# Optimization experiments

Hardware: AMD Instinct MI355X
Metric: run time of the kernel (lower is better)

The kernel has to match this reference:

```python
import jax, jax.numpy as jnp
import numpy as np

N = 20000          # nodes
E = 200000         # edges
IN = 256           # in_channels
OUT = 256          # out_channels (heads * per-head)
H = 2              # heads
C = OUT // 2       # per-head channels (out_channels // 2)
TDIM = 100         # time_enc.out_channels
MSG = 156          # msg_dim
EDGE_DIM = TDIM + MSG  # 256
P = 0.1            # dropout prob


def setup_inputs() -> dict:
    key = jax.random.key(0)
    ks = jax.random.split(key, 20)
    s = 1.0 / np.sqrt(IN)
    se = 1.0 / np.sqrt(EDGE_DIM)
    return {
        "x": jax.random.normal(ks[0], (N, IN), jnp.float32),
        "last_update": jax.random.uniform(ks[1], (N,), jnp.float32) * 100.0,
        "edge_index": jax.random.randint(ks[2], (2, E), 0, N, jnp.int64),
        "t": jax.random.uniform(ks[3], (E,), jnp.float32) * 100.0,
        "msg": jax.random.normal(ks[4], (E, MSG), jnp.float32),
        "u_edge": jax.random.uniform(ks[5], (E,), jnp.float32),
        "u_attn": jax.random.uniform(ks[6], (E, H), jnp.float32),
        # TimeEncoder: cos(Linear(1, TDIM))
        "time_w": jax.random.normal(ks[7], (TDIM,), jnp.float32),
        "time_b": jax.random.normal(ks[8], (TDIM,), jnp.float32) * 0.1,
        # TransformerConv params ([in, out] layout)
        "Wq": jax.random.normal(ks[9], (IN, H * C), jnp.float32) * s,
        "bq": jnp.zeros((H * C,), jnp.float32),
        "Wk": jax.random.normal(ks[10], (IN, H * C), jnp.float32) * s,
        "bk": jnp.zeros((H * C,), jnp.float32),
        "Wv": jax.random.normal(ks[11], (IN, H * C), jnp.float32) * s,
        "bv": jnp.zeros((H * C,), jnp.float32),
        "We": jax.random.normal(ks[12], (EDGE_DIM, H * C), jnp.float32) * se,
        "be": jnp.zeros((H * C,), jnp.float32),
        "Ws": jax.random.normal(ks[13], (IN, H * C), jnp.float32) * s,
        "bs": jnp.zeros((H * C,), jnp.float32),
    }


def reference(x, last_update, edge_index, t, msg, u_edge, u_attn,
              time_w, time_b, Wq, bq, Wk, bk, Wv, bv, We, be, Ws, bs):
    src, dst = edge_index[0], edge_index[1]
    # time encoding of relative time (TGN TimeEncoder: cos(Linear(1, TDIM)))
    rel_t = last_update[src] - t                              # [E]
    rel_enc = jnp.cos(rel_t[:, None] * time_w[None, :] + time_b)  # [E, TDIM]
    edge_attr = jnp.concatenate([rel_enc, msg], axis=-1)      # [E, EDGE_DIM]
    # dropout_adj: drop edges with prob P (no rescale)
    keep = u_edge > P                                         # [E] bool

    q = (x @ Wq + bq).reshape(N, H, C)
    k = (x @ Wk + bk).reshape(N, H, C)
    v = (x @ Wv + bv).reshape(N, H, C)
    e = (edge_attr @ We + be).reshape(E, H, C)

    kj = k[src] + e                                           # [E, H, C]
    alpha = jnp.einsum('ehc,ehc->eh', q[dst], kj) / jnp.sqrt(jnp.float32(C))
    alpha = jnp.where(keep[:, None], alpha, -jnp.inf)
    # segment softmax over incoming edges of each dst node
    m = jax.ops.segment_max(alpha, dst, num_segments=N)       # [N, H]
    m = jnp.where(jnp.isfinite(m), m, 0.0)
    ex = jnp.where(keep[:, None], jnp.exp(alpha - m[dst]), 0.0)
    denom = jax.ops.segment_sum(ex, dst, num_segments=N)      # [N, H]
    attn = ex / (denom[dst] + 1e-16)                          # [E, H]
    # attention dropout (post-softmax, inverted scaling)
    attn = attn * (u_attn > P).astype(attn.dtype) / (1.0 - P)

    msg_out = (v[src] + e) * attn[:, :, None]                 # [E, H, C]
    out = jax.ops.segment_sum(msg_out, dst, num_segments=N).reshape(N, H * C)
    # root/skip connection
    return out + (x @ Ws + bs)
```

## Files before the change

kernel.cpp:

```cpp
#include <hip/hip_runtime.h>

#define NND 20000
#define NE 200000
#define PDROP 0.1f

typedef unsigned short u16;
typedef __bf16 bf16x8 __attribute__((ext_vector_type(8)));
typedef float f32x4 __attribute__((ext_vector_type(4)));

__device__ __forceinline__ float b2f(u16 u) {
  unsigned v = ((unsigned)u) << 16;
  float f;
  __builtin_memcpy(&f, &v, 4);
  return f;
}
__device__ __forceinline__ u16 f2b(float f) {
  unsigned x;
  __builtin_memcpy(&x, &f, 4);
  unsigned r = x + 0x7fffu + ((x >> 16) & 1u);
  return (u16)(r >> 16);
}

__global__ void convert_x(const float* __restrict__ x, u16* __restrict__ xb) {
  int i = blockIdx.x * blockDim.x + threadIdx.x;
  if (i < NND * 256 / 4) {
    float4 v = ((const float4*)x)[i];
    ushort4 o;
    o.x = f2b(v.x); o.y = f2b(v.y); o.z = f2b(v.z); o.w = f2b(v.w);
    ((ushort4*)xb)[i] = o;
  }
}

struct WTArgs {
  const float* W[6];
  u16* WT[6];
};
__global__ void convert_wT(WTArgs a) {
  int gid = blockIdx.x * blockDim.x + threadIdx.x;
  if (gid >= 6 * 65536) return;
  int w = gid >> 16, r = gid & 65535;
  if (w < 5) {
    int n = r >> 8, k = r & 255;
    a.WT[w][n * 256 + k] = f2b(a.W[w][k * 256 + n]);
  } else {
    a.WT[5][r] = f2b(a.W[5][r]);
  }
}

__global__ void zero2(int* __restrict__ cnt, int* __restrict__ cur) {
  int i = blockIdx.x * blockDim.x + threadIdx.x;
  if (i < NND) { cnt[i] = 0; cur[i] = 0; }
}
__global__ void csr_count(const int* __restrict__ ei, int* __restrict__ cnt) {
  int e = blockIdx.x * blockDim.x + threadIdx.x;
  if (e < NE) atomicAdd(&cnt[ei[NE + e]], 1);
}
__global__ __launch_bounds__(1024) void scan_rowptr(const int* __restrict__ cnt,
                                                    int* __restrict__ rowptr) {
  __shared__ int sums[1024];
  const int tid = threadIdx.x;
  const int base = tid * 20;
  int local[20];
  int run = 0;
#pragma unroll
  for (int i = 0; i < 20; i++) {
    int idx = base + i;
    local[i] = run;
    run += (idx < NND) ? cnt[idx] : 0;
  }
  sums[tid] = run;
  __syncthreads();
  for (int off = 1; off < 1024; off <<= 1) {
    int v = (tid >= off) ? sums[tid - off] : 0;
    __syncthreads();
    sums[tid] += v;
    __syncthreads();
  }
  int prev = (tid > 0) ? sums[tid - 1] : 0;
#pragma unroll
  for (int i = 0; i < 20; i++) {
    int idx = base + i;
    if (idx < NND) rowptr[idx] = prev + local[i];
  }
  if (tid == 1023) rowptr[NND] = sums[1023];
}
__global__ void csr_fill(const int* __restrict__ ei,
                         const float* __restrict__ last_update,
                         const float* __restrict__ t,
                         const float* __restrict__ u_edge,
                         const float* __restrict__ u_attn,
                         const int* __restrict__ rowptr, int* __restrict__ cur,
                         int* __restrict__ elist, uint4* __restrict__ recs) {
  int e = blockIdx.x * blockDim.x + threadIdx.x;
  if (e < NE) {
    int s = ei[e];
    int d = ei[NE + e];
    int p = rowptr[d] + atomicAdd(&cur[d], 1);
    elist[p] = e;
    bool keep = u_edge[e] > PDROP;
    float rt = last_update[s] - t[e];
    float2 ua = *(const float2*)&u_attn[(size_t)e * 2];
    uint4 r;
    r.x = (unsigned)s | (keep ? 0u : 0x80000000u);
    r.y = __float_as_uint(rt);
    r.z = __float_as_uint(ua.x > PDROP ? (1.f / 0.9f) : 0.f);
    r.w = __float_as_uint(ua.y > PDROP ? (1.f / 0.9f) : 0.f);
    recs[p] = r;
  }
}

__device__ __forceinline__ void mfma_tile(const u16 (*As)[72], const u16 (*Bs)[72],
                                          f32x4 acc[4][4], int wm, int wn,
                                          int fr, int fg) {
#pragma unroll
  for (int ks = 0; ks < 2; ks++) {
    bf16x8 a[4], b[4];
#pragma unroll
    for (int i = 0; i < 4; i++)
      a[i] = *(const bf16x8*)&As[wm * 64 + i * 16 + fr][ks * 32 + fg * 8];
#pragma unroll
    for (int j = 0; j < 4; j++)
      b[j] = *(const bf16x8*)&Bs[wn * 64 + j * 16 + fr][ks * 32 + fg * 8];
#pragma unroll
    for (int i = 0; i < 4; i++)
#pragma unroll
      for (int j = 0; j < 4; j++)
        acc[i][j] = __builtin_amdgcn_mfma_f32_16x16x32_bf16(a[i], b[j], acc[i][j], 0, 0, 0);
  }
}

struct NodeArgs {
  const u16* BT[4];
  const float* bias[4];
  u16* outb[3];
  float* outf;
};
__global__ __launch_bounds__(256) void gemm_node(const u16* __restrict__ xb,
                                                 NodeArgs args) {
  __shared__ __attribute__((aligned(16))) u16 As[128][72];
  __shared__ __attribute__((aligned(16))) u16 Bs[128][72];
  const int tid = threadIdx.x;
  const int w = blockIdx.y >> 1;
  const int col0 = (blockIdx.y & 1) * 128;
  const int row0 = blockIdx.x * 128;
  const u16* BT = args.BT[w];
  const float* bias = args.bias[w];
  const int wid = tid >> 6, lane = tid & 63;
  const int wm = wid >> 1, wn = wid & 1;
  const int fr = lane & 15, fg = lane >> 4;
  f32x4 acc[4][4] = {};
  for (int k0 = 0; k0 < 256; k0 += 64) {
#pragma unroll
    for (int i = 0; i < 4; i++) {
      int idx = tid + i * 256;
      int row = idx >> 3, vc = idx & 7;
      int g = row0 + row;
      uint4 v = make_uint4(0, 0, 0, 0);
      if (g < NND) v = *(const uint4*)&xb[(size_t)g * 256 + k0 + vc * 8];
      *(uint4*)&As[row][vc * 8] = v;
      *(uint4*)&Bs[row][vc * 8] = *(const uint4*)&BT[(size_t)(col0 + row) * 256 + k0 + vc * 8];
    }
    __syncthreads();
    mfma_tile(As, Bs, acc, wm, wn, fr, fg);
    __syncthreads();
  }
#pragma unroll
  for (int mi = 0; mi < 4; mi++) {
#pragma unroll
    for (int rr = 0; rr < 4; rr++) {
      int grow = row0 + wm * 64 + mi * 16 + fg * 4 + rr;
      if (grow >= NND) continue;
#pragma unroll
      for (int ni = 0; ni < 4; ni++) {
        int gcol = col0 + wn * 64 + ni * 16 + fr;
        float val = acc[mi][ni][rr] + bias[gcol];
        if (w < 3)
          args.outb[w][(size_t)grow * 256 + gcol] = f2b(val);
        else
          args.outf[(size_t)grow * 256 + gcol] = val;
      }
    }
  }
}

__global__ __launch_bounds__(256) void gemm_qwe(const u16* __restrict__ qb,
                                                const u16* __restrict__ Web,
                                                u16* __restrict__ qWeb) {
  __shared__ __attribute__((aligned(16))) u16 As[128][72];
  __shared__ __attribute__((aligned(16))) u16 Bs[128][72];
  const int tid = threadIdx.x;
  const int h = blockIdx.y >> 1;
  const int col0 = (blockIdx.y & 1) * 128;
  const int row0 = blockIdx.x * 128;
  const int wid = tid >> 6, lane = tid & 63;
  const int wm = wid >> 1, wn = wid & 1;
  const int fr = lane & 15, fg = lane >> 4;
  f32x4 acc[4][4] = {};
  for (int k0 = 0; k0 < 128; k0 += 64) {
#pragma unroll
    for (int i = 0; i < 4; i++) {
      int idx = tid + i * 256;
      int row = idx >> 3, vc = idx & 7;
      int g = row0 + row;
      uint4 v = make_uint4(0, 0, 0, 0);
      if (g < NND) v = *(const uint4*)&qb[(size_t)g * 256 + h * 128 + k0 + vc * 8];
      *(uint4*)&As[row][vc * 8] = v;
      *(uint4*)&Bs[row][vc * 8] =
          *(const uint4*)&Web[(size_t)(col0 + row) * 256 + h * 128 + k0 + vc * 8];
    }
    __syncthreads();
    mfma_tile(As, Bs, acc, wm, wn, fr, fg);
    __syncthreads();
  }
#pragma unroll
  for (int mi = 0; mi < 4; mi++) {
#pragma unroll
    for (int rr = 0; rr < 4; rr++) {
      int grow = row0 + wm * 64 + mi * 16 + fg * 4 + rr;
      if (grow >= NND) continue;
#pragma unroll
      for (int ni = 0; ni < 4; ni++) {
        int gj = col0 + wn * 64 + ni * 16 + fr;
        qWeb[(size_t)grow * 512 + h * 256 + gj] = f2b(acc[mi][ni][rr]);
      }
    }
  }
}

__global__ __launch_bounds__(256) void node_fused(
    const u16* __restrict__ qb, const u16* __restrict__ kb,
    const u16* __restrict__ vb, const u16* __restrict__ qWeb,
    const float* __restrict__ msg, const float* __restrict__ tw,
    const float* __restrict__ tb_, const float* __restrict__ be,
    const int* __restrict__ rowptr, const int* __restrict__ elist,
    const uint4* __restrict__ recs, u16* __restrict__ aggb,
    float* __restrict__ out) {
  const int node = (blockIdx.x * blockDim.x + threadIdx.x) >> 6;
  const int lane = threadIdx.x & 63;
  if (node >= NND) return;
  const int beg = rowptr[node], end = rowptr[node + 1];
  const int c0 = lane * 4, hl = lane >> 5;

  ushort4 q4 = *(const ushort4*)&qb[(size_t)node * 256 + c0];
  float qf0 = b2f(q4.x), qf1 = b2f(q4.y), qf2 = b2f(q4.z), qf3 = b2f(q4.w);
  ushort4 w0v = *(const ushort4*)&qWeb[(size_t)node * 512 + c0];
  ushort4 w1v = *(const ushort4*)&qWeb[(size_t)node * 512 + 256 + c0];
  float qw00 = b2f(w0v.x), qw01 = b2f(w0v.y), qw02 = b2f(w0v.z), qw03 = b2f(w0v.w);
  float qw10 = b2f(w1v.x), qw11 = b2f(w1v.y), qw12 = b2f(w1v.z), qw13 = b2f(w1v.w);
  float4 bev = *(const float4*)&be[c0];
  float pb = qf0 * bev.x + qf1 * bev.y + qf2 * bev.z + qf3 * bev.w;
#pragma unroll
  for (int off = 16; off; off >>= 1) pb += __shfl_xor(pb, off);
  float tw0 = 0, tw1 = 0, tw2 = 0, tw3 = 0, tb0 = 0, tb1 = 0, tb2 = 0, tb3 = 0;
  if (c0 < 100) {
    float4 a = *(const float4*)&tw[c0];
    float4 b = *(const float4*)&tb_[c0];
    tw0 = a.x; tw1 = a.y; tw2 = a.z; tw3 = a.w;
    tb0 = b.x; tb1 = b.y; tb2 = b.z; tb3 = b.w;
  }
  const float inv = 0.08838834764831845f;

  float m0 = -INFINITY, m1 = -INFINITY;
  float den0 = 0.f, den1 = 0.f, sw0 = 0.f, sw1 = 0.f;
  float vc0 = 0, vc1 = 0, vc2 = 0, vc3 = 0;
  float g00 = 0, g01 = 0, g02 = 0, g03 = 0;
  float g10 = 0, g11 = 0, g12 = 0, g13 = 0;

  for (int j0 = beg; j0 < end; j0 += 4) {
    float ea[4][4];
    unsigned se[4];
    float rt[4], wk0[4], wk1[4];
    ushort4 k4[4], v4[4];
#pragma unroll
    for (int e = 0; e < 4; ++e) {
      int j = j0 + e;
      int jc = (j < end) ? j : (end - 1);
      uint4 rr = recs[jc];
      bool valid = (j < end);
      se[e] = valid ? rr.x : 0xFFFFFFFFu;
      rt[e] = __uint_as_float(rr.y);
      wk0[e] = valid ? __uint_as_float(rr.z) : 0.f;
      wk1[e] = valid ? __uint_as_float(rr.w) : 0.f;
      int s_ = (int)(rr.x & 0x7fffffffu);
      k4[e] = *(const ushort4*)&kb[(size_t)s_ * 256 + c0];
      v4[e] = *(const ushort4*)&vb[(size_t)s_ * 256 + c0];
      if (c0 >= 100) {
        int eid = elist[jc];
        *(float4*)&ea[e][0] = *(const float4*)&msg[(size_t)eid * 156 + (c0 - 100)];
      }
    }
    if (c0 < 100) {
#pragma unroll
      for (int e = 0; e < 4; ++e) {
        ea[e][0] = __cosf(rt[e] * tw0 + tb0);
        ea[e][1] = __cosf(rt[e] * tw1 + tb1);
        ea[e][2] = __cosf(rt[e] * tw2 + tb2);
        ea[e][3] = __cosf(rt[e] * tw3 + tb3);
      }
    }
    float z[4], pq[4];
#pragma unroll
    for (int e = 0; e < 4; ++e) {
      pq[e] = qf0 * b2f(k4[e].x) + qf1 * b2f(k4[e].y) +
              qf2 * b2f(k4[e].z) + qf3 * b2f(k4[e].w);
      float pe0 = qw00 * ea[e][0] + qw01 * ea[e][1] + qw02 * ea[e][2] + qw03 * ea[e][3];
      float pe1 = qw10 * ea[e][0] + qw11 * ea[e][1] + qw12 * ea[e][2] + qw13 * ea[e][3];
      float y0 = pe0 + __shfl_xor(pe0, 32);
      float y1 = pe1 + __shfl_xor(pe1, 32);
      z[e] = (lane < 32) ? y0 : y1;
    }
#pragma unroll
    for (int off = 16; off; off >>= 1) {
#pragma unroll
      for (int e = 0; e < 4; ++e) {
        z[e] += __shfl_xor(z[e], off);
        pq[e] += __shfl_xor(pq[e], off);
      }
    }
    float a0[4], a1[4];
#pragma unroll
    for (int e = 0; e < 4; ++e) {
      float a = (se[e] < 0x80000000u) ? (pq[e] + z[e] + pb) * inv : -INFINITY;
      float aoth = __shfl_xor(a, 32);
      a0[e] = (lane < 32) ? a : aoth;
      a1[e] = (lane < 32) ? aoth : a;
    }
    float cm0 = fmaxf(fmaxf(a0[0], a0[1]), fmaxf(a0[2], a0[3]));
    float cm1 = fmaxf(fmaxf(a1[0], a1[1]), fmaxf(a1[2], a1[3]));
    if (cm0 > m0) {
      float sc = (m0 > -1e30f) ? __expf(m0 - cm0) : 0.f;
      den0 *= sc; sw0 *= sc;
      g00 *= sc; g01 *= sc; g02 *= sc; g03 *= sc;
      float scv = hl ? 1.f : sc;
      vc0 *= scv; vc1 *= scv; vc2 *= scv; vc3 *= scv;
      m0 = cm0;
    }
    if (cm1 > m1) {
      float sc = (m1 > -1e30f) ? __expf(m1 - cm1) : 0.f;
      den1 *= sc; sw1 *= sc;
      g10 *= sc; g11 *= sc; g12 *= sc; g13 *= sc;
      float scv = hl ? sc : 1.f;
      vc0 *= scv; vc1 *= scv; vc2 *= scv; vc3 *= scv;
      m1 = cm1;
    }
#pragma unroll
    for (int e = 0; e < 4; ++e) {
      float ex0 = (a0[e] > -1e30f) ? __expf(a0[e] - m0) : 0.f;
      float ex1 = (a1[e] > -1e30f) ? __expf(a1[e] - m1) : 0.f;
      den0 += ex0; den1 += ex1;
      float w0 = ex0 * wk0[e], w1 = ex1 * wk1[e];
      float wv = hl ? w1 : w0;
      vc0 += wv * b2f(v4[e].x); vc1 += wv * b2f(v4[e].y);
      vc2 += wv * b2f(v4[e].z); vc3 += wv * b2f(v4[e].w);
      g00 += w0 * ea[e][0]; g01 += w0 * ea[e][1];
      g02 += w0 * ea[e][2]; g03 += w0 * ea[e][3];
      g10 += w1 * ea[e][0]; g11 += w1 * ea[e][1];
      g12 += w1 * ea[e][2]; g13 += w1 * ea[e][3];
      sw0 += w0; sw1 += w1;
    }
  }

  float rden0 = 1.f / (den0 + 1e-16f), rden1 = 1.f / (den1 + 1e-16f);
  float rv = hl ? rden1 : rden0;
  float swv = hl ? sw1 : sw0;
  float4 o = *(float4*)&out[(size_t)node * 256 + c0];
  o.x += (vc0 + swv * bev.x) * rv;
  o.y += (vc1 + swv * bev.y) * rv;
  o.z += (vc2 + swv * bev.z) * rv;
  o.w += (vc3 + swv * bev.w) * rv;
  *(float4*)&out[(size_t)node * 256 + c0] = o;
  ushort4 a0v, a1v;
  a0v.x = f2b(g00 * rden0); a0v.y = f2b(g01 * rden0);
  a0v.z = f2b(g02 * rden0); a0v.w = f2b(g03 * rden0);
  a1v.x = f2b(g10 * rden1); a1v.y = f2b(g11 * rden1);
  a1v.z = f2b(g12 * rden1); a1v.w = f2b(g13 * rden1);
  *(ushort4*)&aggb[(size_t)node * 256 + c0] = a0v;
  *(ushort4*)&aggb[(size_t)(NND + node) * 256 + c0] = a1v;
}

__global__ __launch_bounds__(256) void gemm_final(const u16* __restrict__ aggb,
                                                  const u16* __restrict__ WeT,
                                                  float* __restrict__ out) {
  __shared__ __attribute__((aligned(16))) u16 As[128][72];
  __shared__ __attribute__((aligned(16))) u16 Bs[128][72];
  const int tid = threadIdx.x;
  const int h = blockIdx.y;
  const int row0 = blockIdx.x * 128;
  const u16* A = aggb + (size_t)h * NND * 256;
  const int wid = tid >> 6, lane = tid & 63;
  const int wm = wid >> 1, wn = wid & 1;
  const int fr = lane & 15, fg = lane >> 4;
  f32x4 acc[4][4] = {};
  for (int k0 = 0; k0 < 256; k0 += 64) {
#pragma unroll
    for (int i = 0; i < 4; i++) {
      int idx = tid + i * 256;
      int row = idx >> 3, vc = idx & 7;
      int g = row0 + row;
      uint4 v = make_uint4(0, 0, 0, 0);
      if (g < NND) v = *(const uint4*)&A[(size_t)g * 256 + k0 + vc * 8];
      *(uint4*)&As[row][vc * 8] = v;
      *(uint4*)&Bs[row][vc * 8] =
          *(const uint4*)&WeT[(size_t)(h * 128 + row) * 256 + k0 + vc * 8];
    }
    __syncthreads();
    mfma_tile(As, Bs, acc, wm, wn, fr, fg);
    __syncthreads();
  }
#pragma unroll
  for (int mi = 0; mi < 4; mi++) {
#pragma unroll
    for (int rr = 0; rr < 4; rr++) {
      int grow = row0 + wm * 64 + mi * 16 + fg * 4 + rr;
      if (grow >= NND) continue;
#pragma unroll
      for (int ni = 0; ni < 4; ni++) {
        int gcol = wn * 64 + ni * 16 + fr;
        out[(size_t)grow * 256 + h * 128 + gcol] += acc[mi][ni][rr];
      }
    }
  }
}

extern "C" void kernel_launch(void* const* d_in, const int* in_sizes, int n_in,
                              void* d_out, int out_size, void* d_ws, size_t ws_size,
                              hipStream_t stream) {
  const float* x = (const float*)d_in[0];
  const float* last_update = (const float*)d_in[1];
  const int* ei = (const int*)d_in[2];
  const float* t = (const float*)d_in[3];
  const float* msg = (const float*)d_in[4];
  const float* u_edge = (const float*)d_in[5];
  const float* u_attn = (const float*)d_in[6];
  const float* time_w = (const float*)d_in[7];
  const float* time_b = (const float*)d_in[8];
  const float* Wq = (const float*)d_in[9];
  const float* bq = (const float*)d_in[10];
  const float* Wk = (const float*)d_in[11];
  const float* bk = (const float*)d_in[12];
  const float* Wv = (const float*)d_in[13];
  const float* bv = (const float*)d_in[14];
  const float* We = (const float*)d_in[15];
  const float* be = (const float*)d_in[16];
  const float* Ws = (const float*)d_in[17];
  const float* bs = (const float*)d_in[18];
  float* out = (float*)d_out;

  char* ws = (char*)d_ws;
  u16* xb = (u16*)(ws + 0);
  u16* WT0 = (u16*)(ws + 10240000);
  u16* qb = (u16*)(ws + 11026432);
  u16* kb = (u16*)(ws + 21266432);
  u16* vb = (u16*)(ws + 31506432);
  u16* qWeb = (u16*)(ws + 41746432);
  u16* aggb = (u16*)(ws + 62226432);
  uint4* recs = (uint4*)(ws + 82706432);
  int* cnt = (int*)(ws + 85906432);
  int* cur = (int*)(ws + 85986432);
  int* rowptr = (int*)(ws + 86066432);
  int* elist = (int*)(ws + 86146448);

  zero2<<<(NND + 255) / 256, 256, 0, stream>>>(cnt, cur);
  csr_count<<<(NE + 255) / 256, 256, 0, stream>>>(ei, cnt);
  scan_rowptr<<<1, 1024, 0, stream>>>(cnt, rowptr);
  csr_fill<<<(NE + 255) / 256, 256, 0, stream>>>(ei, last_update, t, u_edge,
                                                 u_attn, rowptr, cur, elist,
                                                 recs);

  WTArgs wa;
  wa.W[0] = Wq; wa.W[1] = Wk; wa.W[2] = Wv; wa.W[3] = Ws; wa.W[4] = We; wa.W[5] = We;
  for (int i = 0; i < 6; i++) wa.WT[i] = WT0 + (size_t)i * 65536;
  convert_wT<<<(6 * 65536 + 255) / 256, 256, 0, stream>>>(wa);
  convert_x<<<(NND * 64 + 255) / 256, 256, 0, stream>>>(x, xb);

  NodeArgs na;
  na.BT[0] = wa.WT[0]; na.BT[1] = wa.WT[1]; na.BT[2] = wa.WT[2]; na.BT[3] = wa.WT[3];
  na.bias[0] = bq; na.bias[1] = bk; na.bias[2] = bv; na.bias[3] = bs;
  na.outb[0] = qb; na.outb[1] = kb; na.outb[2] = vb;
  na.outf = out;
  dim3 gn((NND + 127) / 128, 8);
  gemm_node<<<gn, 256, 0, stream>>>(xb, na);

  dim3 gq((NND + 127) / 128, 4);
  gemm_qwe<<<gq, 256, 0, stream>>>(qb, wa.WT[5], qWeb);

  node_fused<<<(NND + 3) / 4, 256, 0, stream>>>(
      qb, kb, vb, qWeb, msg, time_w, time_b, be, rowptr, elist, recs, aggb,
      out);

  dim3 gf((NND + 127) / 128, 2);
  gemm_final<<<gf, 256, 0, stream>>>(aggb, wa.WT[4], out);
}
```

Measured before the change: 249.1 us.

## Pre-permute msg into CSR order as bf16 for contiguous node_fused reads

```diff
diff --git a/kernel.cpp b/kernel.cpp
--- a/kernel.cpp
+++ b/kernel.cpp
@@ -90,13 +90,13 @@
                          const float* __restrict__ u_edge,
                          const float* __restrict__ u_attn,
                          const int* __restrict__ rowptr, int* __restrict__ cur,
-                         int* __restrict__ elist, uint4* __restrict__ recs) {
+                         int* __restrict__ pos, uint4* __restrict__ recs) {
   int e = blockIdx.x * blockDim.x + threadIdx.x;
   if (e < NE) {
     int s = ei[e];
     int d = ei[NE + e];
     int p = rowptr[d] + atomicAdd(&cur[d], 1);
-    elist[p] = e;
+    pos[e] = p;
     bool keep = u_edge[e] > PDROP;
     float rt = last_update[s] - t[e];
     float2 ua = *(const float2*)&u_attn[(size_t)e * 2];
@@ -107,6 +107,18 @@
     r.w = __float_as_uint(ua.y > PDROP ? (1.f / 0.9f) : 0.f);
     recs[p] = r;
   }
+}
+
+__global__ void msgs_fill(const float* __restrict__ msg,
+                          const int* __restrict__ pos, u16* __restrict__ msgs) {
+  int i = blockIdx.x * blockDim.x + threadIdx.x;
+  if (i >= NE * 39) return;
+  int e = i / 39;
+  int c = (i - e * 39) * 4;
+  float4 v = *(const float4*)&msg[(size_t)e * 156 + c];
+  ushort4 o;
+  o.x = f2b(v.x); o.y = f2b(v.y); o.z = f2b(v.z); o.w = f2b(v.w);
+  *(ushort4*)&msgs[(size_t)pos[e] * 156 + c] = o;
 }
 
 __device__ __forceinline__ void mfma_tile(const u16 (*As)[72], const u16 (*Bs)[72],
@@ -230,11 +242,10 @@
 __global__ __launch_bounds__(256) void node_fused(
     const u16* __restrict__ qb, const u16* __restrict__ kb,
     const u16* __restrict__ vb, const u16* __restrict__ qWeb,
-    const float* __restrict__ msg, const float* __restrict__ tw,
+    const u16* __restrict__ msgs, const float* __restrict__ tw,
     const float* __restrict__ tb_, const float* __restrict__ be,
-    const int* __restrict__ rowptr, const int* __restrict__ elist,
-    const uint4* __restrict__ recs, u16* __restrict__ aggb,
-    float* __restrict__ out) {
+    const int* __restrict__ rowptr, const uint4* __restrict__ recs,
+    u16* __restrict__ aggb, float* __restrict__ out) {
   const int node = (blockIdx.x * blockDim.x + threadIdx.x) >> 6;
   const int lane = threadIdx.x & 63;
   if (node >= NND) return;
@@ -270,7 +281,7 @@
     float ea[4][4];
     unsigned se[4];
     float rt[4], wk0[4], wk1[4];
-    ushort4 k4[4], v4[4];
+    ushort4 k4[4], v4[4], mm4[4];
 #pragma unroll
     for (int e = 0; e < 4; ++e) {
       int j = j0 + e;
@@ -284,10 +295,8 @@
       int s_ = (int)(rr.x & 0x7fffffffu);
       k4[e] = *(const ushort4*)&kb[(size_t)s_ * 256 + c0];
       v4[e] = *(const ushort4*)&vb[(size_t)s_ * 256 + c0];
-      if (c0 >= 100) {
-        int eid = elist[jc];
-        *(float4*)&ea[e][0] = *(const float4*)&msg[(size_t)eid * 156 + (c0 - 100)];
-      }
+      if (c0 >= 100)
+        mm4[e] = *(const ushort4*)&msgs[(size_t)jc * 156 + (c0 - 100)];
     }
     if (c0 < 100) {
 #pragma unroll
@@ -296,6 +305,12 @@
         ea[e][1] = __cosf(rt[e] * tw1 + tb1);
         ea[e][2] = __cosf(rt[e] * tw2 + tb2);
         ea[e][3] = __cosf(rt[e] * tw3 + tb3);
+      }
+    } else {
+#pragma unroll
+      for (int e = 0; e < 4; ++e) {
+        ea[e][0] = b2f(mm4[e].x); ea[e][1] = b2f(mm4[e].y);
+        ea[e][2] = b2f(mm4[e].z); ea[e][3] = b2f(mm4[e].w);
       }
     }
     float z[4], pq[4];
@@ -455,17 +470,19 @@
   u16* qWeb = (u16*)(ws + 41746432);
   u16* aggb = (u16*)(ws + 62226432);
   uint4* recs = (uint4*)(ws + 82706432);
-  int* cnt = (int*)(ws + 85906432);
-  int* cur = (int*)(ws + 85986432);
-  int* rowptr = (int*)(ws + 86066432);
-  int* elist = (int*)(ws + 86146448);
+  u16* msgs = (u16*)(ws + 85906432);
+  int* pos = (int*)(ws + 148306432);
+  int* cnt = (int*)(ws + 149106432);
+  int* cur = (int*)(ws + 149186432);
+  int* rowptr = (int*)(ws + 149266432);
 
   zero2<<<(NND + 255) / 256, 256, 0, stream>>>(cnt, cur);
   csr_count<<<(NE + 255) / 256, 256, 0, stream>>>(ei, cnt);
   scan_rowptr<<<1, 1024, 0, stream>>>(cnt, rowptr);
   csr_fill<<<(NE + 255) / 256, 256, 0, stream>>>(ei, last_update, t, u_edge,
-                                                 u_attn, rowptr, cur, elist,
-                                                 recs);
+                                                 u_attn, rowptr, cur, pos, recs);
+
+  msgs_fill<<<(NE * 39 + 255) / 256, 256, 0, stream>>>(msg, pos, msgs);
 
   WTArgs wa;
   wa.W[0] = Wq; wa.W[1] = Wk; wa.W[2] = Wv; wa.W[3] = Ws; wa.W[4] = We; wa.W[5] = We;
@@ -485,8 +502,7 @@
   gemm_qwe<<<gq, 256, 0, stream>>>(qb, wa.WT[5], qWeb);
 
   node_fused<<<(NND + 3) / 4, 256, 0, stream>>>(
-      qb, kb, vb, qWeb, msg, time_w, time_b, be, rowptr, elist, recs, aggb,
-      out);
+      qb, kb, vb, qWeb, msgs, time_w, time_b, be, rowptr, recs, aggb, out);
 
   dim3 gf((NND + 127) / 128, 2);
   gemm_final<<<gf, 256, 0, stream>>>(aggb, wa.WT[4], out);
```

Result: slower. 256.0 us (+2.7%).
